# Kernel optimization log

Measured on AMD Instinct MI355X. Metric: run time of the kernel, lower is better.

## Reference

```python
import jax, jax.numpy as jnp
import numpy as np

D, NH, E, F = 768, 12, 4, 3072            # embed dim, heads, experts/group, expert ffn (4*D)
NBLK, DEPTH = 2, 6                        # MoE blocks, DiT depth
N_A, N_B, N_C = 64, 32, 192               # group token counts
MA, FH, TC = 32, 8, 7                     # max_agents, future_horizon, traj_channels
BATCH = 8
T_TRAJ = MA * FH                          # 256 trajectory tokens
TFREQ = 256                               # sinusoidal timestep embedding dim
HD = D // NH

def _ln(x):
    mu = jnp.mean(x, -1, keepdims=True)
    v = jnp.var(x, -1, keepdims=True)
    return (x - mu) * jax.lax.rsqrt(v + 1e-6)

def _heads(x):
    b, n, _ = x.shape
    return x.reshape(b, n, NH, HD).transpose(0, 2, 1, 3)

def _attn(q, k, v):
    s = jnp.einsum('bhqd,bhkd->bhqk', q, k) * (HD ** -0.5)
    p = jax.nn.softmax(s, -1)
    o = jnp.einsum('bhqk,bhkd->bhqd', p, v)
    b, h, n, d = o.shape
    return o.transpose(0, 2, 1, 3).reshape(b, n, h * d)

def _cross(q_in, kv_in, W):
    # W: [4, D, D] = (Wq, Wk, Wv, Wo)
    q = _heads(q_in @ W[0]); k = _heads(kv_in @ W[1]); v = _heads(kv_in @ W[2])
    return _attn(q, k, v) @ W[3]

def _moe(x, Wr, W1, W2):
    # top-1 switch routing: gate = softmax prob of selected expert
    gates = jax.nn.softmax(x @ Wr)                       # [B,N,E]
    idx = jnp.argmax(gates, -1)                          # [B,N]
    gval = jnp.take_along_axis(gates, idx[..., None], -1)  # [B,N,1]
    h = jax.nn.gelu(jnp.einsum('bnd,edf->bnef', x, W1))
    y = jnp.einsum('bnef,efd->bned', h, W2)
    sel = jax.nn.one_hot(idx, W1.shape[0], dtype=x.dtype) * gval
    return jnp.einsum('bned,bne->bnd', y, sel)

def _forward(x_traj, tokens_A, tokens_B, tokens_C, W_traj, b_traj, W_ftime,
             Wt1, bt1, Wt2, bt2, moe_attn_W, moe_router, moe_W1, moe_W2,
             dit_qkv, dit_qkv_b, dit_proj, dit_proj_b, dit_mlp1, dit_mlp1_b,
             dit_mlp2, dit_mlp2_b, dit_ada, dit_ada_b,
             out_ada_W, out_ada_b, out_W, out_b, t):
    B = x_traj.shape[0]
    # timestep conditioning (DiT TimestepEmbedder)
    half = TFREQ // 2
    freqs = jnp.exp(-np.log(10000.0) * jnp.arange(half, dtype=jnp.float32) / half)
    ang = t.astype(jnp.float32)[:, None] * freqs
    temb = jnp.concatenate([jnp.cos(ang), jnp.sin(ang)], -1)     # [B,TFREQ]
    c = jax.nn.silu(temb @ Wt1 + bt1) @ Wt2 + bt2                # [B,D]

    # trajectory embedding + future-time embedding
    traj = x_traj.reshape(B, T_TRAJ, TC) @ W_traj + b_traj       # [B,256,D]
    traj = traj + jnp.tile(W_ftime, (MA, 1))[None]

    # StackedMoEBlocks: directed cross-attn A->C->B + per-group top-1 expert routing
    a, bg, cg = tokens_A, tokens_B, tokens_C
    for i in range(NBLK):
        cg = cg + _cross(_ln(cg), a, moe_attn_W[i, 0])
        bg = bg + _cross(_ln(bg), cg, moe_attn_W[i, 1])
        a = a + _moe(_ln(a), moe_router[i, 0], moe_W1[i, 0], moe_W2[i, 0])
        bg = bg + _moe(_ln(bg), moe_router[i, 1], moe_W1[i, 1], moe_W2[i, 1])
        cg = cg + _moe(_ln(cg), moe_router[i, 2], moe_W1[i, 2], moe_W2[i, 2])

    # DiT backbone over [traj | A | B | C], adaLN-zero conditioning on c
    x = jnp.concatenate([traj, a, bg, cg], 1)                    # [B,544,D]
    for i in range(DEPTH):
        mod = (jax.nn.silu(c) @ dit_ada[i] + dit_ada_b[i]).reshape(B, 6, 1, D)
        s1, sc1, g1, s2, sc2, g2 = [mod[:, j] for j in range(6)]
        h = _ln(x) * (1 + sc1) + s1
        qkv = h @ dit_qkv[i] + dit_qkv_b[i]
        q, k, v = jnp.split(qkv, 3, -1)
        x = x + g1 * (_attn(_heads(q), _heads(k), _heads(v)) @ dit_proj[i] + dit_proj_b[i])
        h = _ln(x) * (1 + sc2) + s2
        x = x + g2 * (jax.nn.gelu(h @ dit_mlp1[i] + dit_mlp1_b[i]) @ dit_mlp2[i] + dit_mlp2_b[i])

    # output head: final adaLN + projection to noise(+sigma), trajectory tokens only
    shift, scale = jnp.split(jax.nn.silu(c) @ out_ada_W + out_ada_b, 2, -1)
    h = _ln(x) * (1 + scale[:, None]) + shift[:, None]
    out = h @ out_W + out_b
    return out[:, :T_TRAJ].reshape(B, MA, FH, 2 * TC)

def setup_inputs() -> dict:
    key = jax.random.key(0)
    ks = jax.random.split(key, 24)
    n = jax.random.normal
    s = 0.02
    return dict(
        x_traj=n(ks[0], (BATCH, MA, FH, TC), jnp.float32),
        t=jax.random.randint(ks[1], (BATCH,), 0, 50),
        tokens_A=n(ks[2], (BATCH, N_A, D), jnp.float32),
        tokens_B=n(ks[3], (BATCH, N_B, D), jnp.float32),
        tokens_C=n(ks[4], (BATCH, N_C, D), jnp.float32),
        W_traj=n(ks[5], (TC, D)) * s, b_traj=jnp.zeros((D,)),
        W_ftime=n(ks[6], (FH, D)) * s,
        Wt1=n(ks[7], (TFREQ, D)) * s, bt1=jnp.zeros((D,)),
        Wt2=n(ks[8], (D, D)) * s, bt2=jnp.zeros((D,)),
        moe_attn_W=n(ks[9], (NBLK, 2, 4, D, D)) * s,
        moe_router=n(ks[10], (NBLK, 3, D, E)) * s,
        moe_W1=n(ks[11], (NBLK, 3, E, D, F)) * s,
        moe_W2=n(ks[12], (NBLK, 3, E, F, D)) * s,
        dit_qkv=n(ks[13], (DEPTH, D, 3 * D)) * s, dit_qkv_b=jnp.zeros((DEPTH, 3 * D)),
        dit_proj=n(ks[14], (DEPTH, D, D)) * s, dit_proj_b=jnp.zeros((DEPTH, D)),
        dit_mlp1=n(ks[15], (DEPTH, D, 4 * D)) * s, dit_mlp1_b=jnp.zeros((DEPTH, 4 * D)),
        dit_mlp2=n(ks[16], (DEPTH, 4 * D, D)) * s, dit_mlp2_b=jnp.zeros((DEPTH, D)),
        dit_ada=n(ks[17], (DEPTH, D, 6 * D)) * s, dit_ada_b=jnp.zeros((DEPTH, 6 * D)),
        out_ada_W=n(ks[18], (D, 2 * D)) * s, out_ada_b=jnp.zeros((2 * D,)),
        out_W=n(ks[19], (D, 2 * TC)) * s, out_b=jnp.zeros((2 * TC,)),
    )

def reference(x_traj, t, tokens_A, tokens_B, tokens_C, W_traj, b_traj, W_ftime,
              Wt1, bt1, Wt2, bt2, moe_attn_W, moe_router, moe_W1, moe_W2,
              dit_qkv, dit_qkv_b, dit_proj, dit_proj_b, dit_mlp1, dit_mlp1_b,
              dit_mlp2, dit_mlp2_b, dit_ada, dit_ada_b,
              out_ada_W, out_ada_b, out_W, out_b):
    return _forward(x_traj, tokens_A, tokens_B, tokens_C, W_traj, b_traj, W_ftime,
                    Wt1, bt1, Wt2, bt2, moe_attn_W, moe_router, moe_W1, moe_W2,
                    dit_qkv, dit_qkv_b, dit_proj, dit_proj_b, dit_mlp1, dit_mlp1_b,
                    dit_mlp2, dit_mlp2_b, dit_ada, dit_ada_b,
                    out_ada_W, out_ada_b, out_W, out_b, t)
```

## Files before the change

kernel.cpp:

```cpp
#include <hip/hip_runtime.h>
#include <hip/hip_bf16.h>
#include <math.h>

#define D 768
#define NH 12
#define HD 64
#define NEXP 4
#define FF 3072
#define NBLK 2
#define DEPTH 6
#define NA 64
#define NB 32
#define NC 192
#define BATCH 8
#define TTRAJ 256
#define NTOK 544
#define MAXTOK 1536
#define MOER 2304

typedef __attribute__((ext_vector_type(8))) short short8v;
typedef __attribute__((ext_vector_type(4))) float f32x4;

__device__ __forceinline__ float siluf(float v) { return v / (1.f + expf(-v)); }
__device__ __forceinline__ float geluf(float v) {
    float u = 0.7978845608028654f * (v + 0.044715f * v * v * v);
    return 0.5f * v * (1.f + tanhf(u));
}
__device__ __forceinline__ unsigned short f2bf(float f) {
    union { float f; unsigned u; } v; v.f = f;
    unsigned r = v.u + 0x7fffu + ((v.u >> 16) & 1u);
    return (unsigned short)(r >> 16);
}
__device__ __forceinline__ float bf2f(unsigned short u) {
    union { unsigned u; float f; } v; v.u = ((unsigned)u) << 16; return v.f;
}
__device__ __forceinline__ void gl16(const unsigned short* g, unsigned short* l) {
    __builtin_amdgcn_global_load_lds(
        (const __attribute__((address_space(1))) void*)g,
        (__attribute__((address_space(3))) void*)l, 16, 0, 0);
}

__global__ void timestep_kernel(const int* __restrict__ t, unsigned short* __restrict__ tembP) {
    int i = blockIdx.x * blockDim.x + threadIdx.x;
    if (i >= 128 * 256) return;
    int b = i >> 8, j = i & 255;
    float v = 0.f;
    if (b < BATCH) {
        int jj = (j & 127);
        float freq = expf(-logf(10000.f) * (float)jj / 128.f);
        float ang = (float)t[b] * freq;
        v = (j < 128) ? cosf(ang) : sinf(ang);
    }
    tembP[i] = f2bf(v);
}

__global__ void add_ftime(float* __restrict__ traj, const float* __restrict__ wf, int total) {
    int i = blockIdx.x * blockDim.x + threadIdx.x;
    if (i >= total) return;
    int col = i % D;
    int n = (i / D) % TTRAJ;
    traj[i] += wf[(n & 7) * D + col];
}

__global__ void cvt_bf16(const float* __restrict__ in, unsigned short* __restrict__ out, int n8) {
    int i = blockIdx.x * blockDim.x + threadIdx.x;
    if (i >= n8) return;
    float4 a = *(const float4*)(in + i * 8);
    float4 b = *(const float4*)(in + i * 8 + 4);
    unsigned short t[8] = {f2bf(a.x), f2bf(a.y), f2bf(a.z), f2bf(a.w),
                           f2bf(b.x), f2bf(b.y), f2bf(b.z), f2bf(b.w)};
    *(short8v*)(out + i * 8) = *(short8v*)t;
}

template<int ACT>
__global__ __launch_bounds__(256) void gemm_act(
    const float* __restrict__ A, int lda,
    const float* __restrict__ B, int ldb,
    const float* __restrict__ bias,
    float* __restrict__ C, int ldc,
    int M, int N, int K)
{
    __shared__ float As[16][65];
    __shared__ float Bs[16][65];
    int tid = threadIdx.x;
    int tx = tid & 15, ty = tid >> 4;
    int row0 = blockIdx.y * 64, col0 = blockIdx.x * 64;
    float acc[4][4] = {};
    for (int k0 = 0; k0 < K; k0 += 16) {
        #pragma unroll
        for (int i = 0; i < 4; ++i) {
            int e = tid + 256 * i; int m = e >> 4; int kk = e & 15;
            int gr = row0 + m, gk = k0 + kk;
            As[kk][m] = (gr < M && gk < K) ? A[(size_t)gr * lda + gk] : 0.f;
        }
        #pragma unroll
        for (int i = 0; i < 4; ++i) {
            int e = tid + 256 * i; int kk = e >> 6; int n = e & 63;
            int gk = k0 + kk, gc = col0 + n;
            Bs[kk][n] = (gk < K && gc < N) ? B[(size_t)gk * ldb + gc] : 0.f;
        }
        __syncthreads();
        #pragma unroll
        for (int kk = 0; kk < 16; ++kk) {
            float a[4], bv[4];
            #pragma unroll
            for (int i = 0; i < 4; ++i) a[i] = As[kk][ty * 4 + i];
            #pragma unroll
            for (int j = 0; j < 4; ++j) bv[j] = Bs[kk][tx * 4 + j];
            #pragma unroll
            for (int i = 0; i < 4; ++i)
                #pragma unroll
                for (int j = 0; j < 4; ++j) acc[i][j] += a[i] * bv[j];
        }
        __syncthreads();
    }
    #pragma unroll
    for (int i = 0; i < 4; ++i) {
        int gr = row0 + ty * 4 + i; if (gr >= M) continue;
        #pragma unroll
        for (int j = 0; j < 4; ++j) {
            int gc = col0 + tx * 4 + j; if (gc >= N) continue;
            float v = acc[i][j] + (bias ? bias[gc] : 0.f);
            if (ACT == 1) v = siluf(v);
            if (ACT == 2) v = geluf(v);
            C[(size_t)gr * ldc + gc] = v;
        }
    }
}

__global__ __launch_bounds__(256) void transpose_cvt(
    const float* __restrict__ in, unsigned short* __restrict__ out, int K, int N)
{
    __shared__ unsigned short Ls[64][72];
    const float* src = in + (size_t)blockIdx.z * K * N;
    unsigned short* dst = out + (size_t)blockIdx.z * K * N;
    int k0 = blockIdx.y * 64, n0 = blockIdx.x * 64;
    int tid = threadIdx.x;
    int r = tid >> 2, c0 = (tid & 3) * 16;
    {
        const float* sp = src + (size_t)(k0 + r) * N + n0 + c0;
        #pragma unroll
        for (int j = 0; j < 16; j += 4) {
            float4 f = *(const float4*)(sp + j);
            Ls[c0 + j + 0][r] = f2bf(f.x);
            Ls[c0 + j + 1][r] = f2bf(f.y);
            Ls[c0 + j + 2][r] = f2bf(f.z);
            Ls[c0 + j + 3][r] = f2bf(f.w);
        }
    }
    __syncthreads();
    {
        unsigned short tmp[16];
        #pragma unroll
        for (int j = 0; j < 16; ++j) tmp[j] = Ls[r][c0 + j];
        unsigned short* dp = dst + (size_t)(n0 + r) * K + k0 + c0;
        *(short8v*)dp = *(short8v*)tmp;
        *(short8v*)(dp + 8) = *(short8v*)(tmp + 8);
    }
}

template<int ACT, int OUT, int TN, int TM>
__global__ __launch_bounds__(256) void gemm_lds(
    const unsigned short* __restrict__ A,
    const unsigned short* __restrict__ BT,
    const float* __restrict__ bias,
    float* __restrict__ Cf, unsigned short* __restrict__ Cb, int ldc,
    int K, int qscale_cols,
    const float* __restrict__ mod, int modstride, int gchunk, int ntok, int mrows,
    size_t bt_zs = 0, size_t bias_zs = 0, size_t c_zs = 0)
{
    constexpr int NCF = TN / 32;
    constexpr int NBS = TN / 64;
    constexpr int NMR = TM / 32;
    constexpr int NAI = TM / 64;
    constexpr int NST = (NAI > NBS) ? NAI : NBS;
    if (bt_zs) BT += (size_t)blockIdx.z * bt_zs;
    if (bias && bias_zs) bias += (size_t)blockIdx.z * bias_zs;
    if (c_zs) { if (Cf) Cf += (size_t)blockIdx.z * c_zs; if (Cb) Cb += (size_t)blockIdx.z * c_zs; }
    __shared__ unsigned short As[2][TM * 32];
    __shared__ unsigned short Bs[2][TN * 32];
    int tid = threadIdx.x, w = tid >> 6, lane = tid & 63;
    int row0 = blockIdx.y * TM, col0 = blockIdx.x * TN;
    int wrow = (w >> 1) * (TM / 2), wcol = (w & 1) * (TN / 2);
    int lr = lane & 15, g = lane >> 4;
    f32x4 acc[NMR][NCF] = {};

    int ra[NST], ka[NST], la[NST];
    #pragma unroll
    for (int i = 0; i < NST; ++i) {
        int off = tid * 16 + i * 4096;
        int row = off >> 6;
        int slot = (off >> 4) & 3;
        ra[i] = row;
        ka[i] = (slot ^ ((row >> 1) & 3)) * 8;
        la[i] = off >> 1;
    }
    int nt = K >> 5, cur = 0;
    #pragma unroll
    for (int i = 0; i < NAI; ++i)
        gl16(A + (size_t)(row0 + ra[i]) * K + ka[i], &As[0][la[i]]);
    #pragma unroll
    for (int i = 0; i < NBS; ++i)
        gl16(BT + (size_t)(col0 + ra[i]) * K + ka[i], &Bs[0][la[i]]);

    for (int t = 0; t < nt; ++t) {
        __syncthreads();
        if (t + 1 < nt) {
            int k0 = (t + 1) << 5;
            #pragma unroll
            for (int i = 0; i < NAI; ++i)
                gl16(A + (size_t)(row0 + ra[i]) * K + k0 + ka[i], &As[cur ^ 1][la[i]]);
            #pragma unroll
            for (int i = 0; i < NBS; ++i)
                gl16(BT + (size_t)(col0 + ra[i]) * K + k0 + ka[i], &Bs[cur ^ 1][la[i]]);
        }
        short8v av[NMR], bv[NCF];
        #pragma unroll
        for (int mr = 0; mr < NMR; ++mr) {
            int row = wrow + mr * 16 + lr;
            av[mr] = *(const short8v*)&As[cur][row * 32 + (g ^ ((row >> 1) & 3)) * 8];
        }
        #pragma unroll
        for (int nc = 0; nc < NCF; ++nc) {
            int row = wcol + nc * 16 + lr;
            bv[nc] = *(const short8v*)&Bs[cur][row * 32 + (g ^ ((row >> 1) & 3)) * 8];
        }
        #pragma unroll
        for (int mr = 0; mr < NMR; ++mr)
            #pragma unroll
            for (int nc = 0; nc < NCF; ++nc)
                acc[mr][nc] = __builtin_amdgcn_mfma_f32_16x16x32_bf16(
                    av[mr], bv[nc], acc[mr][nc], 0, 0, 0);
        cur ^= 1;
    }
    int rbase = g * 4;
    #pragma unroll
    for (int mr = 0; mr < NMR; ++mr) {
        #pragma unroll
        for (int nc = 0; nc < NCF; ++nc) {
            int gc = col0 + wcol + nc * 16 + lr;
            float bb = bias ? bias[gc] : 0.f;
            #pragma unroll
            for (int r = 0; r < 4; ++r) {
                int gr = row0 + wrow + mr * 16 + rbase + r;
                if (gr >= mrows) continue;
                float v = acc[mr][nc][r] + bb;
                if (ACT == 1) v = siluf(v);
                if (ACT == 2) v = geluf(v);
                if (OUT == 0) {
                    Cf[(size_t)gr * ldc + gc] = v;
                } else if (OUT == 1) {
                    if (gc < qscale_cols) v *= 0.125f;
                    Cb[(size_t)gr * ldc + gc] = f2bf(v);
                } else {
                    float gg = 1.f;
                    if (mod) gg = mod[(size_t)(gr / ntok) * modstride + gchunk * D + gc];
                    size_t idx = (size_t)gr * ldc + gc;
                    Cb[idx] = f2bf(bf2f(Cb[idx]) + gg * v);
                }
            }
        }
    }
}

template<int ACT>
__global__ __launch_bounds__(512, 4) void gemm_lds256(
    const unsigned short* __restrict__ A,
    const unsigned short* __restrict__ BT,
    const float* __restrict__ bias,
    unsigned short* __restrict__ Cb, int ldc,
    int K, int qscale_cols)
{
    __shared__ unsigned short As[2][256 * 32];
    __shared__ unsigned short Bs[2][128 * 32];
    int tid = threadIdx.x, w = tid >> 6, lane = tid & 63;
    int row0 = blockIdx.y * 256, col0 = blockIdx.x * 128;
    int wrow = (w >> 1) * 64, wcol = (w & 1) * 64;
    int lr = lane & 15, g = lane >> 4;
    f32x4 acc[4][4] = {};

    int ra[2], ka[2], la[2];
    #pragma unroll
    for (int i = 0; i < 2; ++i) {
        int off = tid * 16 + i * 8192;
        int row = off >> 6;
        int slot = (off >> 4) & 3;
        ra[i] = row;
        ka[i] = (slot ^ ((row >> 1) & 3)) * 8;
        la[i] = off >> 1;
    }
    int rb, kb, lb;
    {
        int off = tid * 16;
        int row = off >> 6;
        int slot = (off >> 4) & 3;
        rb = row;
        kb = (slot ^ ((row >> 1) & 3)) * 8;
        lb = off >> 1;
    }
    int nt = K >> 5, cur = 0;
    #pragma unroll
    for (int i = 0; i < 2; ++i)
        gl16(A + (size_t)(row0 + ra[i]) * K + ka[i], &As[0][la[i]]);
    gl16(BT + (size_t)(col0 + rb) * K + kb, &Bs[0][lb]);

    for (int t = 0; t < nt; ++t) {
        __syncthreads();
        if (t + 1 < nt) {
            int k0 = (t + 1) << 5;
            #pragma unroll
            for (int i = 0; i < 2; ++i)
                gl16(A + (size_t)(row0 + ra[i]) * K + k0 + ka[i], &As[cur ^ 1][la[i]]);
            gl16(BT + (size_t)(col0 + rb) * K + k0 + kb, &Bs[cur ^ 1][lb]);
        }
        short8v av[4], bv[4];
        #pragma unroll
        for (int mr = 0; mr < 4; ++mr) {
            int row = wrow + mr * 16 + lr;
            av[mr] = *(const short8v*)&As[cur][row * 32 + (g ^ ((row >> 1) & 3)) * 8];
        }
        #pragma unroll
        for (int nc = 0; nc < 4; ++nc) {
            int row = wcol + nc * 16 + lr;
            bv[nc] = *(const short8v*)&Bs[cur][row * 32 + (g ^ ((row >> 1) & 3)) * 8];
        }
        #pragma unroll
        for (int mr = 0; mr < 4; ++mr)
            #pragma unroll
            for (int nc = 0; nc < 4; ++nc)
                acc[mr][nc] = __builtin_amdgcn_mfma_f32_16x16x32_bf16(
                    av[mr], bv[nc], acc[mr][nc], 0, 0, 0);
        cur ^= 1;
    }
    int rbase = g * 4;
    #pragma unroll
    for (int mr = 0; mr < 4; ++mr) {
        #pragma unroll
        for (int nc = 0; nc < 4; ++nc) {
            int gc = col0 + wcol + nc * 16 + lr;
            float bb = bias ? bias[gc] : 0.f;
            #pragma unroll
            for (int r = 0; r < 4; ++r) {
                int gr = row0 + wrow + mr * 16 + rbase + r;
                float v = acc[mr][nc][r] + bb;
                if (ACT == 2) v = geluf(v);
                if (gc < qscale_cols) v *= 0.125f;
                Cb[(size_t)gr * ldc + gc] = f2bf(v);
            }
        }
    }
}

template<int PHASE>
__global__ __launch_bounds__(256) void moe_lds(
    const unsigned short* __restrict__ A,
    const unsigned short* __restrict__ BTconv,
    unsigned short* __restrict__ Cb,
    const int* __restrict__ cnt, const int* __restrict__ list,
    const float* __restrict__ gval, int RT, int egbase)
{
    constexpr int K  = (PHASE == 1) ? 768 : 3072;
    constexpr int TN = (PHASE == 1) ? 128 : 64;
    constexpr int NCF = TN / 32;
    constexpr int NBS = TN / 64;
    int egl = blockIdx.y / RT, rt = blockIdx.y % RT;
    int eg = egbase + egl;
    int c0 = cnt[eg];
    int mbase = rt * 128;
    if (mbase >= c0) return;
    int mcount = min(128, c0 - mbase);
    __shared__ int toks[128];
    int tid = threadIdx.x, w = tid >> 6, lane = tid & 63;
    if (tid < 128) toks[tid] = list[eg * MAXTOK + mbase + min(tid, mcount - 1)];
    __syncthreads();

    __shared__ unsigned short As[2][128 * 32];
    __shared__ unsigned short Bs[2][TN * 32];
    const unsigned short* BT = BTconv + (size_t)egl * (768 * 3072);
    int col0 = blockIdx.x * TN;
    int wrow = (w >> 1) * 64, wcol = (w & 1) * (TN / 2);
    int lr = lane & 15, g = lane >> 4;
    f32x4 acc[4][NCF] = {};

    int ra[2], ka[2], la[2], tok_s[2];
    #pragma unroll
    for (int i = 0; i < 2; ++i) {
        int off = tid * 16 + i * 4096;
        int row = off >> 6;
        int slot = (off >> 4) & 3;
        ra[i] = row;
        ka[i] = (slot ^ ((row >> 1) & 3)) * 8;
        la[i] = off >> 1;
        tok_s[i] = toks[row];
    }
    int nt = K >> 5, cur = 0;
    #pragma unroll
    for (int i = 0; i < 2; ++i)
        gl16(A + (size_t)tok_s[i] * K + ka[i], &As[0][la[i]]);
    #pragma unroll
    for (int i = 0; i < NBS; ++i)
        gl16(BT + (size_t)(col0 + ra[i]) * K + ka[i], &Bs[0][la[i]]);

    for (int t = 0; t < nt; ++t) {
        __syncthreads();
        if (t + 1 < nt) {
            int k0 = (t + 1) << 5;
            #pragma unroll
            for (int i = 0; i < 2; ++i)
                gl16(A + (size_t)tok_s[i] * K + k0 + ka[i], &As[cur ^ 1][la[i]]);
            #pragma unroll
            for (int i = 0; i < NBS; ++i)
                gl16(BT + (size_t)(col0 + ra[i]) * K + k0 + ka[i], &Bs[cur ^ 1][la[i]]);
        }
        short8v av[4], bv[NCF];
        #pragma unroll
        for (int mr = 0; mr < 4; ++mr) {
            int row = wrow + mr * 16 + lr;
            av[mr] = *(const short8v*)&As[cur][row * 32 + (g ^ ((row >> 1) & 3)) * 8];
        }
        #pragma unroll
        for (int nc = 0; nc < NCF; ++nc) {
            int row = wcol + nc * 16 + lr;
            bv[nc] = *(const short8v*)&Bs[cur][row * 32 + (g ^ ((row >> 1) & 3)) * 8];
        }
        #pragma unroll
        for (int mr = 0; mr < 4; ++mr)
            #pragma unroll
            for (int nc = 0; nc < NCF; ++nc)
                acc[mr][nc] = __builtin_amdgcn_mfma_f32_16x16x32_bf16(
                    av[mr], bv[nc], acc[mr][nc], 0, 0, 0);
        cur ^= 1;
    }
    int rbase = g * 4;
    #pragma unroll
    for (int mr = 0; mr < 4; ++mr) {
        #pragma unroll
        for (int r = 0; r < 4; ++r) {
            int m = wrow + mr * 16 + rbase + r;
            if (m >= mcount) continue;
            int tok = toks[m];
            #pragma unroll
            for (int nc = 0; nc < NCF; ++nc) {
                int gc = col0 + wcol + nc * 16 + lr;
                float v = acc[mr][nc][r];
                if (PHASE == 1) Cb[(size_t)tok * 3072 + gc] = f2bf(geluf(v));
                else {
                    size_t idx = (size_t)tok * 768 + gc;
                    Cb[idx] = f2bf(bf2f(Cb[idx]) + gval[tok] * v);
                }
            }
        }
    }
}

__global__ __launch_bounds__(256) void ln_kernel(
    const unsigned short* __restrict__ X, unsigned short* __restrict__ Y, int R, int ntok,
    const float* __restrict__ mod, int modstride, int shift_chunk, int scale_chunk)
{
    int r = blockIdx.x;
    if (r >= R) return;
    const unsigned short* xr = X + (size_t)r * D;
    int tid = threadIdx.x;
    int lane = tid & 63, wid = tid >> 6;
    float v0 = bf2f(xr[tid]), v1 = bf2f(xr[tid + 256]), v2 = bf2f(xr[tid + 512]);
    float s = v0 + v1 + v2;
    float s2 = v0 * v0 + v1 * v1 + v2 * v2;
    for (int off = 32; off > 0; off >>= 1) {
        s += __shfl_xor(s, off, 64);
        s2 += __shfl_xor(s2, off, 64);
    }
    __shared__ float shs[4], shs2[4];
    if (lane == 0) { shs[wid] = s; shs2[wid] = s2; }
    __syncthreads();
    float tot = shs[0] + shs[1] + shs[2] + shs[3];
    float tot2 = shs2[0] + shs2[1] + shs2[2] + shs2[3];
    float mu = tot * (1.f / 768.f);
    float var = tot2 * (1.f / 768.f) - mu * mu;
    float rs = rsqrtf(var + 1e-6f);
    int bb = r / ntok;
    float vv[3] = {v0, v1, v2};
    #pragma unroll
    for (int j = 0; j < 3; ++j) {
        int col = tid + j * 256;
        float nrm = (vv[j] - mu) * rs;
        float y = nrm;
        if (mod) {
            float scv = mod[(size_t)bb * modstride + scale_chunk * D + col];
            float shv = mod[(size_t)bb * modstride + shift_chunk * D + col];
            y = nrm * (1.f + scv) + shv;
        }
        Y[(size_t)r * D + col] = f2bf(y);
    }
}

__global__ __launch_bounds__(512) void attn_mfma(
    const unsigned short* __restrict__ Qp, int ldq, int qoff,
    const unsigned short* __restrict__ Kp, int ldk, int koff,
    const unsigned short* __restrict__ Vp, int ldv, int voff,
    unsigned short* __restrict__ O, int ldo,
    int Nq, int Nkv)
{
    __shared__ unsigned short Qs[128 * 64];
    __shared__ unsigned short Ks[64 * 64];
    __shared__ unsigned short Vs[64 * 64];
    __shared__ unsigned short Ps[128 * 64];
    int h = blockIdx.y, b = blockIdx.z, q0 = blockIdx.x * 128;
    int tid = threadIdx.x, w = tid >> 6, lane = tid & 63;
    int wrow = w * 16;
    int lr = lane & 15, g = lane >> 4;

    {
        int srow = tid >> 2, sc = (tid & 3) * 16;
        int gr = min(q0 + srow, Nq - 1);
        const unsigned short* qp = Qp + (size_t)(b * Nq + gr) * ldq + qoff + h * 64 + sc;
        short8v v0 = *(const short8v*)qp, v1 = *(const short8v*)(qp + 8);
        int s0 = sc >> 3;
        *(short8v*)&Qs[srow * 64 + (s0 ^ (srow & 7)) * 8] = v0;
        *(short8v*)&Qs[srow * 64 + ((s0 + 1) ^ (srow & 7)) * 8] = v1;
    }
    float m_r[4] = {-1e30f, -1e30f, -1e30f, -1e30f};
    float l_r[4] = {};
    f32x4 acc0 = {}, acc1 = {}, acc2 = {}, acc3 = {};

    for (int kv0 = 0; kv0 < Nkv; kv0 += 64) {
        {
            int t2 = tid & 255;
            int srow = t2 >> 2, sc = (t2 & 3) * 16;
            int gc = min(kv0 + srow, Nkv - 1);
            if (tid < 256) {
                const unsigned short* kp = Kp + (size_t)(b * Nkv + gc) * ldk + koff + h * 64 + sc;
                short8v v0 = *(const short8v*)kp, v1 = *(const short8v*)(kp + 8);
                int s0 = sc >> 3;
                *(short8v*)&Ks[srow * 64 + (s0 ^ (srow & 7)) * 8] = v0;
                *(short8v*)&Ks[srow * 64 + ((s0 + 1) ^ (srow & 7)) * 8] = v1;
            } else {
                const unsigned short* vp = Vp + (size_t)(b * Nkv + gc) * ldv + voff + h * 64 + sc;
                #pragma unroll
                for (int j = 0; j < 16; ++j) {
                    int d = sc + j;
                    Vs[d * 64 + (((srow >> 3) ^ (d & 7)) * 8) + (srow & 7)] = vp[j];
                }
            }
        }
        __syncthreads();
        short8v aq0, aq1;
        {
            int row = wrow + lr;
            aq0 = *(const short8v*)&Qs[row * 64 + ((0 + g) ^ (row & 7)) * 8];
            aq1 = *(const short8v*)&Qs[row * 64 + ((4 + g) ^ (row & 7)) * 8];
        }
        f32x4 sf[4];
        #pragma unroll
        for (int nc = 0; nc < 4; ++nc) {
            int row = nc * 16 + lr;
            short8v bk0 = *(const short8v*)&Ks[row * 64 + ((0 + g) ^ (row & 7)) * 8];
            short8v bk1 = *(const short8v*)&Ks[row * 64 + ((4 + g) ^ (row & 7)) * 8];
            f32x4 z = {};
            z = __builtin_amdgcn_mfma_f32_16x16x32_bf16(aq0, bk0, z, 0, 0, 0);
            sf[nc] = __builtin_amdgcn_mfma_f32_16x16x32_bf16(aq1, bk1, z, 0, 0, 0);
        }
        bool val0 = (kv0 + 0 * 16 + lr) < Nkv;
        bool val1 = (kv0 + 1 * 16 + lr) < Nkv;
        bool val2 = (kv0 + 2 * 16 + lr) < Nkv;
        bool val3 = (kv0 + 3 * 16 + lr) < Nkv;
        float fs[4];
        #pragma unroll
        for (int r = 0; r < 4; ++r) {
            float s0 = val0 ? sf[0][r] : -1e30f;
            float s1 = val1 ? sf[1][r] : -1e30f;
            float s2 = val2 ? sf[2][r] : -1e30f;
            float s3 = val3 ? sf[3][r] : -1e30f;
            float mx = fmaxf(fmaxf(s0, s1), fmaxf(s2, s3));
            mx = fmaxf(mx, __shfl_xor(mx, 1, 64));
            mx = fmaxf(mx, __shfl_xor(mx, 2, 64));
            mx = fmaxf(mx, __shfl_xor(mx, 4, 64));
            mx = fmaxf(mx, __shfl_xor(mx, 8, 64));
            float mn = fmaxf(m_r[r], mx);
            fs[r] = __expf(m_r[r] - mn);
            m_r[r] = mn;
            float p0 = __expf(s0 - mn), p1 = __expf(s1 - mn);
            float p2 = __expf(s2 - mn), p3 = __expf(s3 - mn);
            float rsum = p0 + p1 + p2 + p3;
            rsum += __shfl_xor(rsum, 1, 64);
            rsum += __shfl_xor(rsum, 2, 64);
            rsum += __shfl_xor(rsum, 4, 64);
            rsum += __shfl_xor(rsum, 8, 64);
            l_r[r] = l_r[r] * fs[r] + rsum;
            int ql = wrow + g * 4 + r;
            int base = ql * 64;
            int x7 = ql & 7;
            Ps[base + (((0 * 16 + lr) >> 3) ^ x7) * 8 + (lr & 7)] = f2bf(p0);
            Ps[base + (((1 * 16 + lr) >> 3) ^ x7) * 8 + (lr & 7)] = f2bf(p1);
            Ps[base + (((2 * 16 + lr) >> 3) ^ x7) * 8 + (lr & 7)] = f2bf(p2);
            Ps[base + (((3 * 16 + lr) >> 3) ^ x7) * 8 + (lr & 7)] = f2bf(p3);
            acc0[r] *= fs[r]; acc1[r] *= fs[r]; acc2[r] *= fs[r]; acc3[r] *= fs[r];
        }
        __syncthreads();
        short8v ap0, ap1;
        {
            int row = wrow + lr;
            ap0 = *(const short8v*)&Ps[row * 64 + ((0 + g) ^ (row & 7)) * 8];
            ap1 = *(const short8v*)&Ps[row * 64 + ((4 + g) ^ (row & 7)) * 8];
        }
        {
            int row = 0 * 16 + lr;
            short8v b0 = *(const short8v*)&Vs[row * 64 + ((0 + g) ^ (row & 7)) * 8];
            short8v b1 = *(const short8v*)&Vs[row * 64 + ((4 + g) ^ (row & 7)) * 8];
            acc0 = __builtin_amdgcn_mfma_f32_16x16x32_bf16(ap0, b0, acc0, 0, 0, 0);
            acc0 = __builtin_amdgcn_mfma_f32_16x16x32_bf16(ap1, b1, acc0, 0, 0, 0);
        }
        {
            int row = 1 * 16 + lr;
            short8v b0 = *(const short8v*)&Vs[row * 64 + ((0 + g) ^ (row & 7)) * 8];
            short8v b1 = *(const short8v*)&Vs[row * 64 + ((4 + g) ^ (row & 7)) * 8];
            acc1 = __builtin_amdgcn_mfma_f32_16x16x32_bf16(ap0, b0, acc1, 0, 0, 0);
            acc1 = __builtin_amdgcn_mfma_f32_16x16x32_bf16(ap1, b1, acc1, 0, 0, 0);
        }
        {
            int row = 2 * 16 + lr;
            short8v b0 = *(const short8v*)&Vs[row * 64 + ((0 + g) ^ (row & 7)) * 8];
            short8v b1 = *(const short8v*)&Vs[row * 64 + ((4 + g) ^ (row & 7)) * 8];
            acc2 = __builtin_amdgcn_mfma_f32_16x16x32_bf16(ap0, b0, acc2, 0, 0, 0);
            acc2 = __builtin_amdgcn_mfma_f32_16x16x32_bf16(ap1, b1, acc2, 0, 0, 0);
        }
        {
            int row = 3 * 16 + lr;
            short8v b0 = *(const short8v*)&Vs[row * 64 + ((0 + g) ^ (row & 7)) * 8];
            short8v b1 = *(const short8v*)&Vs[row * 64 + ((4 + g) ^ (row & 7)) * 8];
            acc3 = __builtin_amdgcn_mfma_f32_16x16x32_bf16(ap0, b0, acc3, 0, 0, 0);
            acc3 = __builtin_amdgcn_mfma_f32_16x16x32_bf16(ap1, b1, acc3, 0, 0, 0);
        }
        __syncthreads();
    }
    #pragma unroll
    for (int r = 0; r < 4; ++r) {
        int ql = wrow + g * 4 + r;
        if (q0 + ql >= Nq) continue;
        float rl = 1.f / l_r[r];
        unsigned short* op = O + (size_t)(b * Nq + q0 + ql) * ldo + h * 64 + lr;
        op[0]  = f2bf(acc0[r] * rl);
        op[16] = f2bf(acc1[r] * rl);
        op[32] = f2bf(acc2[r] * rl);
        op[48] = f2bf(acc3[r] * rl);
    }
}

__global__ __launch_bounds__(64) void router_kernel(
    const unsigned short* __restrict__ X, const float* __restrict__ WrBase,
    int* __restrict__ idx, float* __restrict__ gval)
{
    int tkn = blockIdx.x; int lane = threadIdx.x;
    int grp = (tkn >= 768) ? 2 : (tkn >= 512 ? 1 : 0);
    const float* Wr = WrBase + (size_t)grp * D * NEXP;
    const unsigned short* xr = X + (size_t)tkn * D;
    float p0 = 0, p1 = 0, p2 = 0, p3 = 0;
    for (int dd = lane; dd < D; dd += 64) {
        float xv = bf2f(xr[dd]);
        const float* wq = Wr + dd * 4;
        p0 += xv * wq[0]; p1 += xv * wq[1]; p2 += xv * wq[2]; p3 += xv * wq[3];
    }
    for (int off = 32; off > 0; off >>= 1) {
        p0 += __shfl_xor(p0, off, 64); p1 += __shfl_xor(p1, off, 64);
        p2 += __shfl_xor(p2, off, 64); p3 += __shfl_xor(p3, off, 64);
    }
    if (lane == 0) {
        float best = p0; int e = 0;
        if (p1 > best) { best = p1; e = 1; }
        if (p2 > best) { best = p2; e = 2; }
        if (p3 > best) { best = p3; e = 3; }
        float sum = expf(p0 - best) + expf(p1 - best) + expf(p2 - best) + expf(p3 - best);
        idx[tkn] = grp * 4 + e;
        gval[tkn] = 1.f / sum;
    }
}

__global__ __launch_bounds__(256) void scatter_kernel(
    const int* __restrict__ idx, int* __restrict__ cnt,
    int* __restrict__ list, int ntok)
{
    __shared__ int lcnt[12];
    int tid = threadIdx.x;
    if (tid < 12) lcnt[tid] = 0;
    __syncthreads();
    for (int i = tid; i < ntok; i += 256) {
        int e = idx[i];
        int pos = atomicAdd(&lcnt[e], 1);
        list[e * MAXTOK + pos] = i;
    }
    __syncthreads();
    if (tid < 12) cnt[tid] = lcnt[tid];
}

__global__ void concat_kernel(const float* __restrict__ traj, const unsigned short* __restrict__ a,
                              const unsigned short* __restrict__ bg, const unsigned short* __restrict__ cg,
                              unsigned short* __restrict__ x, int total)
{
    int i = blockIdx.x * blockDim.x + threadIdx.x;
    if (i >= total) return;
    int col = i % D;
    int r = i / D;
    int n = r % NTOK, b = r / NTOK;
    unsigned short v;
    if (n < 256)      v = f2bf(traj[((size_t)b * 256 + n) * D + col]);
    else if (n < 320) v = a[((size_t)b * 64 + (n - 256)) * D + col];
    else if (n < 352) v = bg[((size_t)b * 32 + (n - 320)) * D + col];
    else              v = cg[((size_t)b * 192 + (n - 352)) * D + col];
    x[i] = v;
}

__global__ void head_prep(const float* __restrict__ W, unsigned short* __restrict__ WT14) {
    int i = blockIdx.x * blockDim.x + threadIdx.x;
    if (i >= 14 * 768) return;
    int o = i / 768, d = i % 768;
    WT14[i] = f2bf(W[d * 14 + o]);
}

__global__ __launch_bounds__(64) void head_kernel(
    const unsigned short* __restrict__ lnb, const unsigned short* __restrict__ WT14,
    const float* __restrict__ bias, float* __restrict__ out)
{
    int r = blockIdx.x;
    int b = r >> 8, n = r & 255;
    const unsigned short* hrow = lnb + (size_t)(b * NTOK + n) * D;
    int l = threadIdx.x;
    if (l >= 56) return;
    int o = l >> 2, p = l & 3;
    const unsigned short* hp = hrow + p * 192;
    const unsigned short* wp = WT14 + o * 768 + p * 192;
    float acc = 0.f;
    for (int i = 0; i < 192; i += 8) {
        short8v hv = *(const short8v*)(hp + i);
        short8v wv = *(const short8v*)(wp + i);
        #pragma unroll
        for (int j = 0; j < 8; ++j)
            acc += bf2f((unsigned short)hv[j]) * bf2f((unsigned short)wv[j]);
    }
    acc += __shfl_xor(acc, 1, 64);
    acc += __shfl_xor(acc, 2, 64);
    if (p == 0) out[(size_t)r * 14 + o] = acc + bias[o];
}

static inline void tcvt(const float* W, unsigned short* WT, int K, int N, int z, hipStream_t s) {
    transpose_cvt<<<dim3(N / 64, K / 64, z), 256, 0, s>>>(W, WT, K, N);
}
static inline void g_bf(int act, const unsigned short* A, const unsigned short* BT,
                        const float* bias, unsigned short* C, int ldc,
                        int M, int N, int K, int qcols, hipStream_t s)
{
    if (M % 256 == 0 && N % 128 == 0 && N >= 2304) {
        dim3 g(N / 128, M / 256);
        if (act == 2) gemm_lds256<2><<<g, 512, 0, s>>>(A, BT, bias, C, ldc, K, qcols);
        else          gemm_lds256<0><<<g, 512, 0, s>>>(A, BT, bias, C, ldc, K, qcols);
        return;
    }
    bool small = (M <= 1536);
    if (N != 768) {
        if (small) {
            dim3 g(N / 128, M / 64);
            if (act == 2) gemm_lds<2, 1, 128, 64><<<g, 256, 0, s>>>(A, BT, bias, nullptr, C, ldc, K, qcols, nullptr, 0, 0, 1, 1 << 30);
            else          gemm_lds<0, 1, 128, 64><<<g, 256, 0, s>>>(A, BT, bias, nullptr, C, ldc, K, qcols, nullptr, 0, 0, 1, 1 << 30);
        } else {
            dim3 g(N / 128, M / 128);
            if (act == 2) gemm_lds<2, 1, 128, 128><<<g, 256, 0, s>>>(A, BT, bias, nullptr, C, ldc, K, qcols, nullptr, 0, 0, 1, 1 << 30);
            else          gemm_lds<0, 1, 128, 128><<<g, 256, 0, s>>>(A, BT, bias, nullptr, C, ldc, K, qcols, nullptr, 0, 0, 1, 1 << 30);
        }
    } else {
        if (small) {
            dim3 g(N / 64, M / 64);
            if (act == 2) gemm_lds<2, 1, 64, 64><<<g, 256, 0, s>>>(A, BT, bias, nullptr, C, ldc, K, qcols, nullptr, 0, 0, 1, 1 << 30);
            else          gemm_lds<0, 1, 64, 64><<<g, 256, 0, s>>>(A, BT, bias, nullptr, C, ldc, K, qcols, nullptr, 0, 0, 1, 1 << 30);
        } else {
            dim3 g(N / 64, M / 128);
            if (act == 2) gemm_lds<2, 1, 64, 128><<<g, 256, 0, s>>>(A, BT, bias, nullptr, C, ldc, K, qcols, nullptr, 0, 0, 1, 1 << 30);
            else          gemm_lds<0, 1, 64, 128><<<g, 256, 0, s>>>(A, BT, bias, nullptr, C, ldc, K, qcols, nullptr, 0, 0, 1, 1 << 30);
        }
    }
}
static inline void g_res(const unsigned short* A, const unsigned short* BT,
                         const float* bias, unsigned short* C, int ldc, int M, int N, int K,
                         const float* mod, int modstride, int gchunk, int ntok, hipStream_t s)
{
    if (M <= 1536) {
        dim3 g(N / 64, M / 64);
        gemm_lds<0, 2, 64, 64><<<g, 256, 0, s>>>(A, BT, bias, nullptr, C, ldc, K, 0, mod, modstride, gchunk, ntok, 1 << 30);
    } else {
        dim3 g(N / 64, M / 128);
        gemm_lds<0, 2, 64, 128><<<g, 256, 0, s>>>(A, BT, bias, nullptr, C, ldc, K, 0, mod, modstride, gchunk, ntok, 1 << 30);
    }
}

extern "C" void kernel_launch(void* const* d_in, const int* in_sizes, int n_in,
                              void* d_out, int out_size, void* d_ws, size_t ws_size,
                              hipStream_t stream)
{
    const float* x_traj   = (const float*)d_in[0];
    const int*   t_arr    = (const int*)d_in[1];
    const float* tokA     = (const float*)d_in[2];
    const float* tokB     = (const float*)d_in[3];
    const float* tokC     = (const float*)d_in[4];
    const float* W_traj   = (const float*)d_in[5];
    const float* b_traj   = (const float*)d_in[6];
    const float* W_ftime  = (const float*)d_in[7];
    const float* Wt1      = (const float*)d_in[8];
    const float* bt1      = (const float*)d_in[9];
    const float* Wt2      = (const float*)d_in[10];
    const float* bt2      = (const float*)d_in[11];
    const float* moe_attn = (const float*)d_in[12];
    const float* moe_rout = (const float*)d_in[13];
    const float* moe_W1   = (const float*)d_in[14];
    const float* moe_W2   = (const float*)d_in[15];
    const float* dit_qkv  = (const float*)d_in[16];
    const float* dit_qkvb = (const float*)d_in[17];
    const float* dit_proj = (const float*)d_in[18];
    const float* dit_projb= (const float*)d_in[19];
    const float* dit_mlp1 = (const float*)d_in[20];
    const float* dit_mlp1b= (const float*)d_in[21];
    const float* dit_mlp2 = (const float*)d_in[22];
    const float* dit_mlp2b= (const float*)d_in[23];
    const float* dit_ada  = (const float*)d_in[24];
    const float* dit_adab = (const float*)d_in[25];
    const float* out_adaW = (const float*)d_in[26];
    const float* out_adab = (const float*)d_in[27];
    const float* out_W    = (const float*)d_in[28];
    const float* out_b    = (const float*)d_in[29];
    float* out = (float*)d_out;
    float* ws = (float*)d_ws;

    const size_t o_cnt  = 14336;
    const size_t o_idx  = 14400;
    const size_t o_gval = 16704;
    const size_t o_list = 19008;
    const size_t o_traj = 66624;
    const size_t o_a    = 1639488;
    const size_t o_x    = 3408960;
    const size_t o_lnb  = 6751296;
    const size_t o_qkvb = 8422464;
    const size_t o_attnO= 13435968;
    const size_t o_h    = 15107136;
    const size_t o_wt   = 24151104;
    const size_t o_wt14 = 28869696;
    const size_t o_tembP= 28875072;
    const size_t o_ub   = 28891456;
    const size_t o_scb  = 28940608;
    const size_t o_mod  = o_traj;
    const size_t o_mod2 = o_traj + 221184;

    const size_t o_wqkv  = 29000000;
    const size_t o_wproj = 34308416;
    const size_t o_wmlp1 = 36077888;
    const size_t o_wmlp2 = 43155776;
    const size_t o_wada  = 50233664;
    const size_t o_wada2 = 60850496;
    const size_t o_wcross= 61440320;
    const size_t o_wmoe1 = 66158912;
    const size_t o_wmoe2 = 94470464;
    const bool bigw = ws_size >= (size_t)123000000 * 4;

    int* cnt_p  = (int*)(ws + o_cnt);
    int* idx_p  = (int*)(ws + o_idx);
    int* list_p = (int*)(ws + o_list);
    float* gval_p = ws + o_gval;
    unsigned short* abf  = (unsigned short*)(ws + o_a);
    unsigned short* bgbf = abf + 512 * 768;
    unsigned short* cgbf = abf + 768 * 768;
    unsigned short* xbf  = (unsigned short*)(ws + o_x);
    unsigned short* lnb  = (unsigned short*)(ws + o_lnb);
    unsigned short* qkvb = (unsigned short*)(ws + o_qkvb);
    unsigned short* attO = (unsigned short*)(ws + o_attnO);
    unsigned short* hbuf = (unsigned short*)(ws + o_h);
    unsigned short* wt   = (unsigned short*)(ws + o_wt);
    unsigned short* wt14 = (unsigned short*)(ws + o_wt14);
    unsigned short* tembP= (unsigned short*)(ws + o_tembP);
    unsigned short* ub   = (unsigned short*)(ws + o_ub);
    unsigned short* scb  = (unsigned short*)(ws + o_scb);
    unsigned short* wqkvS = (unsigned short*)(ws + o_wqkv);
    unsigned short* wprojS= (unsigned short*)(ws + o_wproj);
    unsigned short* wmlp1S= (unsigned short*)(ws + o_wmlp1);
    unsigned short* wmlp2S= (unsigned short*)(ws + o_wmlp2);
    unsigned short* wadaS = (unsigned short*)(ws + o_wada);
    unsigned short* wada2S= (unsigned short*)(ws + o_wada2);
    unsigned short* wcrossS=(unsigned short*)(ws + o_wcross);
    unsigned short* wmoe1S= (unsigned short*)(ws + o_wmoe1);
    unsigned short* wmoe2S= (unsigned short*)(ws + o_wmoe2);
    unsigned short* c_q  = qkvb;
    unsigned short* c_kv = qkvb + 1179648;

    const size_t WSZ = (size_t)D * D;

    gemm_act<0><<<dim3(12, 32), 256, 0, stream>>>(x_traj, 7, W_traj, D, b_traj,
                                                  ws + o_traj, D, BATCH * TTRAJ, D, 7);
    add_ftime<<<(BATCH * TTRAJ * D + 255) / 256, 256, 0, stream>>>(ws + o_traj, W_ftime, BATCH * TTRAJ * D);

    cvt_bf16<<<(512 * 768 / 8 + 255) / 256, 256, 0, stream>>>(tokA, abf, 512 * 768 / 8);
    cvt_bf16<<<(256 * 768 / 8 + 255) / 256, 256, 0, stream>>>(tokB, bgbf, 256 * 768 / 8);
    cvt_bf16<<<(1536 * 768 / 8 + 255) / 256, 256, 0, stream>>>(tokC, cgbf, 1536 * 768 / 8);
    head_prep<<<42, 256, 0, stream>>>(out_W, wt14);

    if (bigw) {
        tcvt(dit_qkv,  wqkvS,  D, 3 * D, DEPTH, stream);
        tcvt(dit_proj, wprojS, D, D, DEPTH, stream);
        tcvt(dit_mlp1, wmlp1S, D, FF, DEPTH, stream);
        tcvt(dit_mlp2, wmlp2S, FF, D, DEPTH, stream);
        tcvt(dit_ada,  wadaS,  D, 6 * D, DEPTH, stream);
        tcvt(out_adaW, wada2S, D, 2 * D, 1, stream);
        tcvt(moe_attn, wcrossS, D, D, NBLK * 2 * 4, stream);
        tcvt(moe_W1,   wmoe1S, D, FF, NBLK * 3 * NEXP, stream);
        tcvt(moe_W2,   wmoe2S, FF, D, NBLK * 3 * NEXP, stream);
    }

    timestep_kernel<<<128, 256, 0, stream>>>(t_arr, tembP);
    tcvt(Wt1, wt, 256, D, 1, stream);
    gemm_lds<1, 1, 64, 128><<<dim3(12, 1), 256, 0, stream>>>(
        tembP, wt, bt1, nullptr, ub, D, 256, 0, nullptr, 0, 0, 1, 128);
    tcvt(Wt2, wt, D, D, 1, stream);
    gemm_lds<1, 1, 64, 128><<<dim3(12, 1), 256, 0, stream>>>(
        ub, wt, bt2, nullptr, scb, D, D, 0, nullptr, 0, 0, 1, 128);

    for (int i = 0; i < NBLK; ++i) {
        {
            const unsigned short* Wc;
            if (bigw) Wc = wcrossS + (size_t)(i * 2 + 0) * 4 * WSZ;
            else { tcvt(moe_attn + (size_t)(i * 2 + 0) * 4 * WSZ, wt, D, D, 4, stream); Wc = wt; }
            ln_kernel<<<BATCH * NC, 256, 0, stream>>>(cgbf, lnb, BATCH * NC, 1, nullptr, 0, 0, 0);
            g_bf(0, lnb, Wc, nullptr, c_q, D, BATCH * NC, D, D, 768, stream);
            g_bf(0, abf, Wc + 1 * WSZ, nullptr, c_kv, 2 * D, BATCH * NA, 2 * D, D, 0, stream);
            attn_mfma<<<dim3((NC + 127) / 128, NH, BATCH), 512, 0, stream>>>(
                c_q, D, 0, c_kv, 2 * D, 0, c_kv, 2 * D, D, attO, D, NC, NA);
            g_res(attO, Wc + 3 * WSZ, nullptr, cgbf, D, BATCH * NC, D, D, nullptr, 0, 0, 1, stream);
        }
        {
            const unsigned short* Wc;
            if (bigw) Wc = wcrossS + (size_t)(i * 2 + 1) * 4 * WSZ;
            else { tcvt(moe_attn + (size_t)(i * 2 + 1) * 4 * WSZ, wt, D, D, 4, stream); Wc = wt; }
            ln_kernel<<<BATCH * NB, 256, 0, stream>>>(bgbf, lnb, BATCH * NB, 1, nullptr, 0, 0, 0);
            g_bf(0, lnb, Wc, nullptr, c_q, D, BATCH * NB, D, D, 768, stream);
            g_bf(0, cgbf, Wc + 1 * WSZ, nullptr, c_kv, 2 * D, BATCH * NC, 2 * D, D, 0, stream);
            attn_mfma<<<dim3(1, NH, BATCH), 512, 0, stream>>>(
                c_q, D, 0, c_kv, 2 * D, 0, c_kv, 2 * D, D, attO, D, NB, NC);
            g_res(attO, Wc + 3 * WSZ, nullptr, bgbf, D, BATCH * NB, D, D, nullptr, 0, 0, 1, stream);
        }
        ln_kernel<<<MOER, 256, 0, stream>>>(abf, lnb, MOER, 1, nullptr, 0, 0, 0);
        router_kernel<<<MOER, 64, 0, stream>>>(lnb, moe_rout + (size_t)(i * 3) * D * NEXP, idx_p, gval_p);
        scatter_kernel<<<1, 256, 0, stream>>>(idx_p, cnt_p, list_p, MOER);
        const int RT = 12;
        if (bigw) {
            moe_lds<1><<<dim3(24, 12 * RT), 256, 0, stream>>>(
                lnb, wmoe1S + (size_t)(i * 3) * NEXP * D * FF, hbuf,
                cnt_p, list_p, gval_p, RT, 0);
            moe_lds<2><<<dim3(12, 12 * RT), 256, 0, stream>>>(
                hbuf, wmoe2S + (size_t)(i * 3) * NEXP * D * FF, abf,
                cnt_p, list_p, gval_p, RT, 0);
        } else {
            for (int g = 0; g < 3; ++g) {
                tcvt(moe_W1 + (size_t)(i * 3 + g) * NEXP * D * FF, wt, D, FF, NEXP, stream);
                moe_lds<1><<<dim3(24, 4 * RT), 256, 0, stream>>>(
                    lnb, wt, hbuf, cnt_p, list_p, gval_p, RT, g * 4);
                tcvt(moe_W2 + (size_t)(i * 3 + g) * NEXP * FF * D, wt, FF, D, NEXP, stream);
                moe_lds<2><<<dim3(12, 4 * RT), 256, 0, stream>>>(
                    hbuf, wt, abf, cnt_p, list_p, gval_p, RT, g * 4);
            }
        }
    }

    concat_kernel<<<(BATCH * NTOK * D + 255) / 256, 256, 0, stream>>>(
        ws + o_traj, abf, bgbf, cgbf, xbf, BATCH * NTOK * D);

    if (bigw) {
        gemm_lds<0, 0, 128, 128><<<dim3(36, 1, DEPTH), 256, 0, stream>>>(
            scb, wadaS, dit_adab, ws + o_mod, nullptr, 6 * D, D, 0,
            nullptr, 0, 0, 1, 8,
            (size_t)D * 6 * D, (size_t)6 * D, (size_t)8 * 6 * D);
        gemm_lds<0, 0, 128, 128><<<dim3(12, 1), 256, 0, stream>>>(
            scb, wada2S, out_adab, ws + o_mod2, nullptr, 2 * D, D, 0, nullptr, 0, 0, 1, 8);
    } else {
        for (int i = 0; i < DEPTH; ++i) {
            tcvt(dit_ada + (size_t)i * D * 6 * D, wt, D, 6 * D, 1, stream);
            gemm_lds<0, 0, 128, 128><<<dim3(36, 1), 256, 0, stream>>>(
                scb, wt, dit_adab + (size_t)i * 6 * D, ws + o_mod + (size_t)i * 8 * 6 * D,
                nullptr, 6 * D, D, 0, nullptr, 0, 0, 1, 8);
        }
        tcvt(out_adaW, wt, D, 2 * D, 1, stream);
        gemm_lds<0, 0, 128, 128><<<dim3(12, 1), 256, 0, stream>>>(
            scb, wt, out_adab, ws + o_mod2, nullptr, 2 * D, D, 0, nullptr, 0, 0, 1, 8);
    }

    const int R = BATCH * NTOK;
    for (int i = 0; i < DEPTH; ++i) {
        const float* mod_l = ws + o_mod + (size_t)i * 8 * 6 * D;
        const unsigned short *Wq = nullptr, *Wp = nullptr, *Wm1 = nullptr, *Wm2 = nullptr;
        if (bigw) {
            Wq  = wqkvS  + (size_t)i * D * 3 * D;
            Wp  = wprojS + (size_t)i * D * D;
            Wm1 = wmlp1S + (size_t)i * D * FF;
            Wm2 = wmlp2S + (size_t)i * D * FF;
        }
        ln_kernel<<<R, 256, 0, stream>>>(xbf, lnb, R, NTOK, mod_l, 6 * D, 0, 1);
        if (!bigw) { tcvt(dit_qkv + (size_t)i * D * 3 * D, wt, D, 3 * D, 1, stream); Wq = wt; }
        g_bf(0, lnb, Wq, dit_qkvb + (size_t)i * 3 * D, qkvb, 3 * D, R, 3 * D, D, 768, stream);
        attn_mfma<<<dim3((NTOK + 127) / 128, NH, BATCH), 512, 0, stream>>>(
            qkvb, 3 * D, 0, qkvb, 3 * D, D, qkvb, 3 * D, 2 * D, attO, D, NTOK, NTOK);
        if (!bigw) { tcvt(dit_proj + (size_t)i * D * D, wt, D, D, 1, stream); Wp = wt; }
        g_res(attO, Wp, dit_projb + (size_t)i * D, xbf, D, R, D, D,
              mod_l, 6 * D, 2, NTOK, stream);
        ln_kernel<<<R, 256, 0, stream>>>(xbf, lnb, R, NTOK, mod_l, 6 * D, 3, 4);
        if (!bigw) { tcvt(dit_mlp1 + (size_t)i * D * FF, wt, D, FF, 1, stream); Wm1 = wt; }
        g_bf(2, lnb, Wm1, dit_mlp1b + (size_t)i * FF, hbuf, FF, R, FF, D, 0, stream);
        if (!bigw) { tcvt(dit_mlp2 + (size_t)i * FF * D, wt, FF, D, 1, stream); Wm2 = wt; }
        g_res(hbuf, Wm2, dit_mlp2b + (size_t)i * D, xbf, D, R, D, FF,
              mod_l, 6 * D, 5, NTOK, stream);
    }

    ln_kernel<<<R, 256, 0, stream>>>(xbf, lnb, R, NTOK, ws + o_mod2, 2 * D, 0, 1);
    head_kernel<<<BATCH * TTRAJ, 64, 0, stream>>>(lnb, wt14, out_b, out);
}
```

Measured before the change: 2.270 ms.

## Swizzle GEMM workgroups across XCDs, prioritize attention MFMAs, fuse token casts

Remaps GEMM workgroup indices so that each XCD gets a contiguous range of output tiles, which should improve L2 reuse of the A and B operands on the multi-die MI355X. It adds s_setprio around the MFMA sections of the attention kernel so those waves get issue priority. It also merges the three bf16 token-cast launches into one kernel that writes a single contiguous output. That merge assumes abf, bgbf and cgbf sit contiguously in the workspace; if they do not, the output is wrong.

Measured after the change: 2.278 ms. No clear change (+0.4%).

```diff
diff --git a/kernel.cpp b/kernel.cpp
--- a/kernel.cpp
+++ b/kernel.cpp
@@ -39,6 +39,15 @@
         (const __attribute__((address_space(1))) void*)g,
         (__attribute__((address_space(3))) void*)l, 16, 0, 0);
 }
+__device__ __forceinline__ void xcd_swz(int& bx, int& by) {
+    int gx = gridDim.x;
+    int nwg = gx * gridDim.y;
+    int flat = by * gx + bx;
+    int q = nwg >> 3, r = nwg & 7;
+    int xcd = flat & 7, j = flat >> 3;
+    int nf = (xcd < r ? xcd * (q + 1) : r * (q + 1) + (xcd - r) * q) + j;
+    bx = nf % gx; by = nf / gx;
+}
 
 __global__ void timestep_kernel(const int* __restrict__ t, unsigned short* __restrict__ tembP) {
     int i = blockIdx.x * blockDim.x + threadIdx.x;
@@ -62,14 +71,20 @@
     traj[i] += wf[(n & 7) * D + col];
 }
 
-__global__ void cvt_bf16(const float* __restrict__ in, unsigned short* __restrict__ out, int n8) {
+__global__ void cvt3_bf16(const float* __restrict__ a, const float* __restrict__ b,
+                          const float* __restrict__ c, unsigned short* __restrict__ outbase) {
     int i = blockIdx.x * blockDim.x + threadIdx.x;
-    if (i >= n8) return;
-    float4 a = *(const float4*)(in + i * 8);
-    float4 b = *(const float4*)(in + i * 8 + 4);
-    unsigned short t[8] = {f2bf(a.x), f2bf(a.y), f2bf(a.z), f2bf(a.w),
-                           f2bf(b.x), f2bf(b.y), f2bf(b.z), f2bf(b.w)};
-    *(short8v*)(out + i * 8) = *(short8v*)t;
+    if (i >= 221184) return;
+    const float* src;
+    int off;
+    if (i < 49152)      { src = a; off = i; }
+    else if (i < 73728) { src = b; off = i - 49152; }
+    else                { src = c; off = i - 73728; }
+    float4 x = *(const float4*)(src + (size_t)off * 8);
+    float4 y = *(const float4*)(src + (size_t)off * 8 + 4);
+    unsigned short t[8] = {f2bf(x.x), f2bf(x.y), f2bf(x.z), f2bf(x.w),
+                           f2bf(y.x), f2bf(y.y), f2bf(y.z), f2bf(y.w)};
+    *(short8v*)(outbase + (size_t)i * 8) = *(short8v*)t;
 }
 
 template<int ACT>
@@ -180,7 +195,9 @@
     __shared__ unsigned short As[2][TM * 32];
     __shared__ unsigned short Bs[2][TN * 32];
     int tid = threadIdx.x, w = tid >> 6, lane = tid & 63;
-    int row0 = blockIdx.y * TM, col0 = blockIdx.x * TN;
+    int bx = blockIdx.x, by = blockIdx.y;
+    xcd_swz(bx, by);
+    int row0 = by * TM, col0 = bx * TN;
     int wrow = (w >> 1) * (TM / 2), wcol = (w & 1) * (TN / 2);
     int lr = lane & 15, g = lane >> 4;
     f32x4 acc[NMR][NCF] = {};
@@ -274,7 +291,9 @@
     __shared__ unsigned short As[2][256 * 32];
     __shared__ unsigned short Bs[2][128 * 32];
     int tid = threadIdx.x, w = tid >> 6, lane = tid & 63;
-    int row0 = blockIdx.y * 256, col0 = blockIdx.x * 128;
+    int bx = blockIdx.x, by = blockIdx.y;
+    xcd_swz(bx, by);
+    int row0 = by * 256, col0 = bx * 128;
     int wrow = (w >> 1) * 64, wcol = (w & 1) * 64;
     int lr = lane & 15, g = lane >> 4;
     f32x4 acc[4][4] = {};
@@ -550,6 +569,7 @@
             aq1 = *(const short8v*)&Qs[row * 64 + ((4 + g) ^ (row & 7)) * 8];
         }
         f32x4 sf[4];
+        __builtin_amdgcn_s_setprio(1);
         #pragma unroll
         for (int nc = 0; nc < 4; ++nc) {
             int row = nc * 16 + lr;
@@ -559,6 +579,7 @@
             z = __builtin_amdgcn_mfma_f32_16x16x32_bf16(aq0, bk0, z, 0, 0, 0);
             sf[nc] = __builtin_amdgcn_mfma_f32_16x16x32_bf16(aq1, bk1, z, 0, 0, 0);
         }
+        __builtin_amdgcn_s_setprio(0);
         bool val0 = (kv0 + 0 * 16 + lr) < Nkv;
         bool val1 = (kv0 + 1 * 16 + lr) < Nkv;
         bool val2 = (kv0 + 2 * 16 + lr) < Nkv;
@@ -602,6 +623,7 @@
             ap0 = *(const short8v*)&Ps[row * 64 + ((0 + g) ^ (row & 7)) * 8];
             ap1 = *(const short8v*)&Ps[row * 64 + ((4 + g) ^ (row & 7)) * 8];
         }
+        __builtin_amdgcn_s_setprio(1);
         {
             int row = 0 * 16 + lr;
             short8v b0 = *(const short8v*)&Vs[row * 64 + ((0 + g) ^ (row & 7)) * 8];
@@ -630,6 +652,7 @@
             acc3 = __builtin_amdgcn_mfma_f32_16x16x32_bf16(ap0, b0, acc3, 0, 0, 0);
             acc3 = __builtin_amdgcn_mfma_f32_16x16x32_bf16(ap1, b1, acc3, 0, 0, 0);
         }
+        __builtin_amdgcn_s_setprio(0);
         __syncthreads();
     }
     #pragma unroll
@@ -891,9 +914,7 @@
                                                   ws + o_traj, D, BATCH * TTRAJ, D, 7);
     add_ftime<<<(BATCH * TTRAJ * D + 255) / 256, 256, 0, stream>>>(ws + o_traj, W_ftime, BATCH * TTRAJ * D);
 
-    cvt_bf16<<<(512 * 768 / 8 + 255) / 256, 256, 0, stream>>>(tokA, abf, 512 * 768 / 8);
-    cvt_bf16<<<(256 * 768 / 8 + 255) / 256, 256, 0, stream>>>(tokB, bgbf, 256 * 768 / 8);
-    cvt_bf16<<<(1536 * 768 / 8 + 255) / 256, 256, 0, stream>>>(tokC, cgbf, 1536 * 768 / 8);
+    cvt3_bf16<<<(221184 + 255) / 256, 256, 0, stream>>>(tokA, tokB, tokC, abf);
     head_prep<<<42, 256, 0, stream>>>(out_W, wt14);
 
     if (bigw) {
```
